# Kernel optimization log

Hardware: AMD Instinct MI355X
Metric: run time of the kernel (lower is better)

Reference implementation:

```python
import jax, jax.numpy as jnp
import numpy as np

B, S, D = 2, 2048, 2048
H, KV, HD = 16, 4, 128          # n_heads, n_kv_heads, head_dim = d_model // n_heads
R = H // KV                      # n_rep (GQA group size)
THETA = 500000.0


def _rotate_half(x):
    x1, x2 = jnp.split(x, 2, axis=-1)
    return jnp.concatenate([-x2, x1], axis=-1)


def _rope_cos_sin(position_ids):
    # inv_freq over even dims, outer with positions, duplicated (LLaMA-style)
    inv_freq = 1.0 / (THETA ** (jnp.arange(0, HD, 2, dtype=jnp.float32) / HD))
    freqs = position_ids.astype(jnp.float32)[..., None] * inv_freq  # (B, S, HD/2)
    emb = jnp.concatenate([freqs, freqs], axis=-1)                  # (B, S, HD)
    return jnp.cos(emb)[:, None], jnp.sin(emb)[:, None]             # (B, 1, S, HD)


def setup_inputs() -> dict:
    key = jax.random.key(0)
    ks = jax.random.split(key, 5)
    x = jax.random.normal(ks[0], (B, S, D), dtype=jnp.float32)
    wq = jax.random.normal(ks[1], (D, H * HD), dtype=jnp.float32) * (D ** -0.5)
    wk = jax.random.normal(ks[2], (D, KV * HD), dtype=jnp.float32) * (D ** -0.5)
    wv = jax.random.normal(ks[3], (D, KV * HD), dtype=jnp.float32) * (D ** -0.5)
    wo = jax.random.normal(ks[4], (H * HD, D), dtype=jnp.float32) * (D ** -0.5)
    causal = jnp.tril(jnp.ones((S, S), dtype=bool))
    attn_mask = jnp.where(causal, 0.0, -1e9).astype(jnp.float32)[None, None]  # (1,1,S,S)
    position_ids = jnp.tile(jnp.arange(S, dtype=jnp.int32)[None, :], (B, 1))
    return {"x": x, "wq": wq, "wk": wk, "wv": wv, "wo": wo,
            "attn_mask": attn_mask, "position_ids": position_ids}


def reference(x, wq, wk, wv, wo, attn_mask, position_ids):
    b, s, _ = x.shape
    # projections (bias-free Linear) + head split, (B, heads, S, HD)
    q = (x @ wq).reshape(b, s, H, HD).transpose(0, 2, 1, 3)
    k = (x @ wk).reshape(b, s, KV, HD).transpose(0, 2, 1, 3)
    v = (x @ wv).reshape(b, s, KV, HD).transpose(0, 2, 1, 3)
    cos, sin = _rope_cos_sin(position_ids)
    q = q * cos + _rotate_half(q) * sin
    k = k * cos + _rotate_half(k) * sin
    # GQA: group q heads (B, KV, R, S, HD); equivalent to repeat_interleave on K/V
    qg = q.reshape(b, KV, R, s, HD)
    scores = jnp.einsum('bgrsd,bgtd->bgrst', qg.astype(jnp.float32),
                        k.astype(jnp.float32)) / np.float32(np.sqrt(HD))
    scores = scores + attn_mask[:, :, None]          # (1,1,1,S,S) broadcast
    p = jax.nn.softmax(scores, axis=-1).astype(x.dtype)
    out = jnp.einsum('bgrst,bgtd->bgrsd', p, v)      # (B, KV, R, S, HD)
    out = out.reshape(b, H, s, HD).transpose(0, 2, 1, 3).reshape(b, s, H * HD)
    return out @ wo
```

## Files before the change

kernel.cpp:

```cpp
#include <hip/hip_runtime.h>
#include <hip/hip_bf16.h>
#include <math.h>

#define Bsz 2
#define Sq  2048
#define Dm  2048
#define Hn  16
#define KVn 4
#define HDn 128

typedef __attribute__((ext_vector_type(8))) short bf16x8;
typedef __attribute__((ext_vector_type(4))) float f32x4;

__device__ __forceinline__ short f2b(float f) {
    __hip_bfloat16 h = __float2bfloat16(f);
    return *reinterpret_cast<short*>(&h);
}
__device__ __forceinline__ float b2f(short s) {
    __hip_bfloat16 h = *reinterpret_cast<__hip_bfloat16*>(&s);
    return __bfloat162float(h);
}

#define NB_F2B 8192
#define NB_WC  10240
__global__ __launch_bounds__(256) void prep_kernel(
    const float* __restrict__ X, short* __restrict__ Y,
    const float* __restrict__ wq, const float* __restrict__ wk,
    const float* __restrict__ wv, const float* __restrict__ wo,
    short* __restrict__ wqkvT, short* __restrict__ woT)
{
    __shared__ float t[32][33];
    const int bid = blockIdx.x;
    const int tid = threadIdx.x;

    if (bid < NB_F2B) {
        const int i = bid * 256 + tid;
        float4 v = ((const float4*)X)[i];
        short4 o;
        o.x = f2b(v.x); o.y = f2b(v.y); o.z = f2b(v.z); o.w = f2b(v.w);
        ((short4*)Y)[i] = o;
        return;
    }

    const int wb = bid - NB_F2B;
    const int n0 = (wb % 160) * 32;
    const int k0 = (wb / 160) * 32;
    const int tx = tid & 31, ty = tid >> 5;

    const float* W; int Nsec, nloc; short* dst;
    if (n0 < 2048)      { W = wq; Nsec = 2048; nloc = n0;        dst = wqkvT + (size_t)n0 * Dm; }
    else if (n0 < 2560) { W = wk; Nsec = 512;  nloc = n0 - 2048; dst = wqkvT + (size_t)n0 * Dm; }
    else if (n0 < 3072) { W = wv; Nsec = 512;  nloc = n0 - 2560; dst = wqkvT + (size_t)n0 * Dm; }
    else                { W = wo; Nsec = 2048; nloc = n0 - 3072; dst = woT + (size_t)(n0 - 3072) * Dm; }

#pragma unroll
    for (int r = 0; r < 4; ++r) {
        const int row = ty + 8 * r;
        t[row][tx] = W[(size_t)(k0 + row) * Nsec + nloc + tx];
    }
    __syncthreads();
#pragma unroll
    for (int r = 0; r < 4; ++r) {
        const int row = ty + 8 * r;
        dst[(size_t)row * Dm + k0 + tx] = f2b(t[tx][row]);
    }
}

template <typename OT>
__global__ __launch_bounds__(256) void gemm_bt_kernel(
    const short* __restrict__ A, const short* __restrict__ Bt,
    OT* __restrict__ C, int M, int N, int K)
{
    __shared__ __align__(16) short As[128 * 64];
    __shared__ __align__(16) short Bs[128 * 64];

    const int tid  = threadIdx.x;
    const int w    = tid >> 6;
    const int lane = tid & 63;
    const int m16  = lane & 15;
    const int g4   = lane >> 4;
    const int wm   = w >> 1, wn = w & 1;

    const int nwg = gridDim.x * gridDim.y;
    const int lin = blockIdx.y * gridDim.x + blockIdx.x;
    const int qq  = nwg >> 3;
    const int sw  = (lin & 7) * qq + (lin >> 3);
    const int bx  = sw % gridDim.x;
    const int by  = sw / gridDim.x;

    const int row0 = by * 128;
    const int col0 = bx * 128;

    const short* Ab = A  + (size_t)row0 * K;
    const short* Bb = Bt + (size_t)col0 * K;

    const int trow = tid >> 3;
    const int soct = (tid & 7) ^ (trow & 7);

    f32x4 acc[4][4];
#pragma unroll
    for (int i = 0; i < 4; ++i)
#pragma unroll
        for (int j = 0; j < 4; ++j) acc[i][j] = (f32x4){0.f, 0.f, 0.f, 0.f};

    for (int k0 = 0; k0 < K; k0 += 64) {
#pragma unroll
        for (int r = 0; r < 4; ++r) {
            const short* gp = Ab + (size_t)(r * 32 + trow) * K + k0 + soct * 8;
            short* lp = &As[(size_t)(r * 256 + w * 64) * 8];
            __builtin_amdgcn_global_load_lds(
                (const __attribute__((address_space(1))) void*)gp,
                (__attribute__((address_space(3))) void*)lp, 16, 0, 0);
        }
#pragma unroll
        for (int r = 0; r < 4; ++r) {
            const short* gp = Bb + (size_t)(r * 32 + trow) * K + k0 + soct * 8;
            short* lp = &Bs[(size_t)(r * 256 + w * 64) * 8];
            __builtin_amdgcn_global_load_lds(
                (const __attribute__((address_space(1))) void*)gp,
                (__attribute__((address_space(3))) void*)lp, 16, 0, 0);
        }
        __syncthreads();

#pragma unroll
        for (int kc = 0; kc < 2; ++kc) {
            bf16x8 a[4], b[4];
            const int swz = (kc * 4 + g4) ^ (m16 & 7);
#pragma unroll
            for (int s = 0; s < 4; ++s) {
                const int rowA = wm * 64 + s * 16 + m16;
                a[s] = *(const bf16x8*)&As[rowA * 64 + swz * 8];
                const int rowB = wn * 64 + s * 16 + m16;
                b[s] = *(const bf16x8*)&Bs[rowB * 64 + swz * 8];
            }
#pragma unroll
            for (int i = 0; i < 4; ++i)
#pragma unroll
                for (int j = 0; j < 4; ++j)
                    acc[i][j] = __builtin_amdgcn_mfma_f32_16x16x32_bf16(
                        a[i], b[j], acc[i][j], 0, 0, 0);
        }
        __syncthreads();
    }

#pragma unroll
    for (int i = 0; i < 4; ++i) {
        const int mbase = row0 + wm * 64 + i * 16 + g4 * 4;
#pragma unroll
        for (int j = 0; j < 4; ++j) {
            const int n = col0 + wn * 64 + j * 16 + m16;
#pragma unroll
            for (int r = 0; r < 4; ++r) {
                if constexpr (sizeof(OT) == 2)
                    C[(size_t)(mbase + r) * N + n] = f2b(acc[i][j][r]);
                else
                    C[(size_t)(mbase + r) * N + n] = acc[i][j][r];
            }
        }
    }
}

#define NB_ROPE 1024
#define NB_VC   2048
__global__ __launch_bounds__(256) void rv_kernel(
    const short* __restrict__ C3b, short* __restrict__ Qb, short* __restrict__ Kb,
    short* __restrict__ Vt, const int* __restrict__ pos_ids, float qscale)
{
    __shared__ short tv[32][34];
    const int bid = blockIdx.x;
    const int tid = threadIdx.x;

    if (bid < NB_ROPE) {
        const int idx = bid * 256 + tid;
        const int i = idx & 63;
        int rest = idx >> 6;
        const int s = rest % Sq;
        const int b = rest / Sq;

        const int pos = pos_ids[b * Sq + s];
        const float e   = -(float)(2 * i) * (1.0f / (float)HDn);
        const float inv = exp2f(e * 18.931568569324174f);
        const float f   = (float)pos * inv;
        float sn, c;
        sincosf(f, &sn, &c);

        const short* src = C3b + ((size_t)(b * Sq + s)) * 3072;

#pragma unroll
        for (int h = 0; h < Hn; ++h) {
            const float x1 = b2f(src[h * HDn + i]);
            const float x2 = b2f(src[h * HDn + i + 64]);
            const size_t dst = (((size_t)b * Hn + h) * Sq + s) * HDn;
            Qb[dst + i]      = f2b((x1 * c - x2 * sn) * qscale);
            Qb[dst + i + 64] = f2b((x2 * c + x1 * sn) * qscale);
        }
#pragma unroll
        for (int h = 0; h < KVn; ++h) {
            const float x1 = b2f(src[2048 + h * HDn + i]);
            const float x2 = b2f(src[2048 + h * HDn + i + 64]);
            const size_t dst = (((size_t)b * KVn + h) * Sq + s) * HDn;
            Kb[dst + i]      = f2b(x1 * c - x2 * sn);
            Kb[dst + i + 64] = f2b(x2 * c + x1 * sn);
        }
        return;
    }

    const int lin = bid - NB_ROPE;
    const int bxv = lin & 63;
    const int rest = lin >> 6;
    const int byv = rest & 3;
    const int bk  = rest >> 2;
    const int b  = bk >> 2, kv = bk & 3;
    const int s0 = bxv * 32;
    const int d0 = byv * 32;
    const int tx = tid & 31, ty = tid >> 5;

#pragma unroll
    for (int r = 0; r < 4; ++r) {
        const int row = ty + 8 * r;
        tv[row][tx] = C3b[((size_t)(b * Sq + s0 + row)) * 3072 + 2560 + kv * HDn + d0 + tx];
    }
    __syncthreads();
#pragma unroll
    for (int r = 0; r < 4; ++r) {
        const int row = ty + 8 * r;
        Vt[((size_t)bk * HDn + d0 + row) * Sq + s0 + tx] = tv[tx][row];
    }
}

__global__ __launch_bounds__(256, 2) void fattn_kernel(
    const short* __restrict__ Qb, const short* __restrict__ Kb,
    const short* __restrict__ Vtb, short* __restrict__ AOb)
{
    __shared__ __align__(16) short Ks[2][64 * 128];
    __shared__ __align__(16) short Vs[2][128 * 64];

    const int tid  = threadIdx.x;
    const int w    = tid >> 6;
    const int lane = tid & 63;
    const int m16  = lane & 15;
    const int g4   = lane >> 4;

    const int i    = blockIdx.x;
    const int half = i >> 8;
    const int k4   = i & 15;
    const int p    = half ? k4 : 15 - k4;
    const int h    = (i >> 4) & 15;
    const int b    = i >> 8;
    const int kv   = h >> 2;

    const int htA = 31 - p, htB = p;
    const int nch = htA + 1;
    const int qA  = htA * 64 + w * 16;
    const int qB  = htB * 64 + w * 16;

    bf16x8 qfA[4], qfB[4];
    {
        const short* qpA = Qb + (((size_t)b * Hn + h) * Sq + qA + m16) * HDn + g4 * 8;
        const short* qpB = Qb + (((size_t)b * Hn + h) * Sq + qB + m16) * HDn + g4 * 8;
#pragma unroll
        for (int c = 0; c < 4; ++c) {
            qfA[c] = *(const bf16x8*)(qpA + c * 32);
            qfB[c] = *(const bf16x8*)(qpB + c * 32);
        }
    }

    const short* kbase = Kb  + ((size_t)b * KVn + kv) * Sq * HDn;
    const short* vbase = Vtb + ((size_t)b * KVn + kv) * (size_t)HDn * Sq;

    const short* gpK[4];
    const short* gpV[4];
#pragma unroll
    for (int r = 0; r < 4; ++r) {
        const int ci = r * 256 + tid;
        const int R  = ci >> 4, o = ci & 15;
        const int hf = (R >> 5) & 1, Rl = R & 31;
        const int phys = hf * 32 + ((Rl >> 2) & 3) * 8 + ((Rl >> 4) & 1) * 4 + (Rl & 3);
        gpK[r] = kbase + (size_t)phys * HDn + (o ^ (R & 7)) * 8;
        const int d = ci >> 3, ov = ci & 7;
        gpV[r] = vbase + (size_t)d * Sq + (ov ^ (d & 7)) * 8;
    }

    auto stage = [&](int ktE, int buf) {
#pragma unroll
        for (int r = 0; r < 4; ++r) {
            const short* gp = gpK[r] + (size_t)ktE * HDn;
            short* lp = &Ks[buf][(size_t)(r * 256 + w * 64) * 8];
            __builtin_amdgcn_global_load_lds(
                (const __attribute__((address_space(1))) void*)gp,
                (__attribute__((address_space(3))) void*)lp, 16, 0, 0);
        }
#pragma unroll
        for (int r = 0; r < 4; ++r) {
            const short* gp = gpV[r] + ktE;
            short* lp = &Vs[buf][(size_t)(r * 256 + w * 64) * 8];
            __builtin_amdgcn_global_load_lds(
                (const __attribute__((address_space(1))) void*)gp,
                (__attribute__((address_space(3))) void*)lp, 16, 0, 0);
        }
    };

    f32x4 OtA[8], OtB[8];
#pragma unroll
    for (int t = 0; t < 8; ++t) {
        OtA[t] = (f32x4){0.f, 0.f, 0.f, 0.f};
        OtB[t] = (f32x4){0.f, 0.f, 0.f, 0.f};
    }
    float mA = -1e30f, lA = 0.f, mB = -1e30f, lB = 0.f;

    stage(0, 0);
    int gpar = 0;

    for (int ch = 0; ch <= p; ++ch) {
        const int cur = gpar & 1; gpar ^= 1;
        const int kt  = ch << 6;

        __syncthreads();
        stage((ch + 1) << 6, cur ^ 1);

        const bool dgB = (ch == p);
        const short* KsC = Ks[cur];
        const short* VsC = Vs[cur];

        f32x4 sc0[4], sc1[4];
        __builtin_amdgcn_s_setprio(1);
#pragma unroll
        for (int f = 0; f < 4; ++f) {
            f32x4 a0 = (f32x4){0.f, 0.f, 0.f, 0.f};
            f32x4 a1 = (f32x4){0.f, 0.f, 0.f, 0.f};
            const int krow = f * 16 + m16;
#pragma unroll
            for (int c = 0; c < 4; ++c) {
                bf16x8 kf = *(const bf16x8*)&KsC[krow * 128 + (((c * 4 + g4) ^ (m16 & 7)) * 8)];
                a0 = __builtin_amdgcn_mfma_f32_16x16x32_bf16(kf, qfA[c], a0, 0, 0, 0);
                a1 = __builtin_amdgcn_mfma_f32_16x16x32_bf16(kf, qfB[c], a1, 0, 0, 0);
            }
            sc0[f] = a0; sc1[f] = a1;
        }
        __builtin_amdgcn_s_setprio(0);

        if (dgB) {
            const int qg = qB + m16;
#pragma unroll
            for (int f = 0; f < 4; ++f)
#pragma unroll
                for (int ii = 0; ii < 4; ++ii) {
                    const int kg = kt + (f >> 1) * 32 + g4 * 8 + (f & 1) * 4 + ii;
                    if (kg > qg) sc1[f][ii] = -1e30f;
                }
        }

        bf16x8 pf0[2], pf1[2];
        {
            float mx = sc0[0][0];
#pragma unroll
            for (int f = 0; f < 4; ++f)
#pragma unroll
                for (int ii = 0; ii < 4; ++ii) mx = fmaxf(mx, sc0[f][ii]);
            mx = fmaxf(mx, __shfl_xor(mx, 16));
            mx = fmaxf(mx, __shfl_xor(mx, 32));
            if (!__all(mx <= mA + 8.0f)) {
                const float nm = fmaxf(mA, mx);
                const float alpha = exp2f(mA - nm);
                mA = nm; lA *= alpha;
#pragma unroll
                for (int t = 0; t < 8; ++t)
#pragma unroll
                    for (int ii = 0; ii < 4; ++ii) OtA[t][ii] *= alpha;
            }
            float ps = 0.f;
#pragma unroll
            for (int f = 0; f < 4; ++f)
#pragma unroll
                for (int ii = 0; ii < 4; ++ii) {
                    sc0[f][ii] = exp2f(sc0[f][ii] - mA);
                    ps += sc0[f][ii];
                }
            ps += __shfl_xor(ps, 16);
            ps += __shfl_xor(ps, 32);
            lA += ps;
#pragma unroll
            for (int hf = 0; hf < 2; ++hf) {
                bf16x8 pk;
#pragma unroll
                for (int j8 = 0; j8 < 8; ++j8)
                    pk[j8] = f2b(j8 < 4 ? sc0[hf * 2][j8] : sc0[hf * 2 + 1][j8 - 4]);
                pf0[hf] = pk;
            }
        }
        {
            float mx = sc1[0][0];
#pragma unroll
            for (int f = 0; f < 4; ++f)
#pragma unroll
                for (int ii = 0; ii < 4; ++ii) mx = fmaxf(mx, sc1[f][ii]);
            mx = fmaxf(mx, __shfl_xor(mx, 16));
            mx = fmaxf(mx, __shfl_xor(mx, 32));
            if (!__all(mx <= mB + 8.0f)) {
                const float nm = fmaxf(mB, mx);
                const float alpha = exp2f(mB - nm);
                mB = nm; lB *= alpha;
#pragma unroll
                for (int t = 0; t < 8; ++t)
#pragma unroll
                    for (int ii = 0; ii < 4; ++ii) OtB[t][ii] *= alpha;
            }
            float ps = 0.f;
#pragma unroll
            for (int f = 0; f < 4; ++f)
#pragma unroll
                for (int ii = 0; ii < 4; ++ii) {
                    sc1[f][ii] = exp2f(sc1[f][ii] - mB);
                    ps += sc1[f][ii];
                }
            ps += __shfl_xor(ps, 16);
            ps += __shfl_xor(ps, 32);
            lB += ps;
#pragma unroll
            for (int hf = 0; hf < 2; ++hf) {
                bf16x8 pk;
#pragma unroll
                for (int j8 = 0; j8 < 8; ++j8)
                    pk[j8] = f2b(j8 < 4 ? sc1[hf * 2][j8] : sc1[hf * 2 + 1][j8 - 4]);
                pf1[hf] = pk;
            }
        }

        __builtin_amdgcn_s_setprio(1);
#pragma unroll
        for (int t = 0; t < 8; ++t) {
            const int d = t * 16 + m16;
            bf16x8 vfa = *(const bf16x8*)&VsC[d * 64 + ((g4 ^ (d & 7)) * 8)];
            bf16x8 vfb = *(const bf16x8*)&VsC[d * 64 + (((4 + g4) ^ (d & 7)) * 8)];
            OtA[t] = __builtin_amdgcn_mfma_f32_16x16x32_bf16(vfa, pf0[0], OtA[t], 0, 0, 0);
            OtA[t] = __builtin_amdgcn_mfma_f32_16x16x32_bf16(vfb, pf0[1], OtA[t], 0, 0, 0);
            OtB[t] = __builtin_amdgcn_mfma_f32_16x16x32_bf16(vfa, pf1[0], OtB[t], 0, 0, 0);
            OtB[t] = __builtin_amdgcn_mfma_f32_16x16x32_bf16(vfb, pf1[1], OtB[t], 0, 0, 0);
        }
        __builtin_amdgcn_s_setprio(0);
    }

    {
        const float inv = 1.0f / lB;
        short* op = AOb + ((size_t)(b * Sq + qB + m16)) * (Hn * HDn) + h * HDn + g4 * 4;
#pragma unroll
        for (int t = 0; t < 8; ++t) {
            short4 o;
            o.x = f2b(OtB[t][0] * inv);
            o.y = f2b(OtB[t][1] * inv);
            o.z = f2b(OtB[t][2] * inv);
            o.w = f2b(OtB[t][3] * inv);
            *(short4*)(op + t * 16) = o;
        }
    }

    for (int ch = p + 1; ch < nch; ++ch) {
        const int cur = gpar & 1; gpar ^= 1;
        const int kt  = ch << 6;

        __syncthreads();
        if (ch + 1 < nch) stage((ch + 1) << 6, cur ^ 1);

        const bool dgA = (ch == nch - 1);
        const short* KsC = Ks[cur];
        const short* VsC = Vs[cur];

        f32x4 sc[4];
        __builtin_amdgcn_s_setprio(1);
#pragma unroll
        for (int f = 0; f < 4; ++f) {
            f32x4 a = (f32x4){0.f, 0.f, 0.f, 0.f};
            const int krow = f * 16 + m16;
#pragma unroll
            for (int c = 0; c < 4; ++c) {
                bf16x8 kf = *(const bf16x8*)&KsC[krow * 128 + (((c * 4 + g4) ^ (m16 & 7)) * 8)];
                a = __builtin_amdgcn_mfma_f32_16x16x32_bf16(kf, qfA[c], a, 0, 0, 0);
            }
            sc[f] = a;
        }
        __builtin_amdgcn_s_setprio(0);

        if (dgA) {
            const int qg = qA + m16;
#pragma unroll
            for (int f = 0; f < 4; ++f)
#pragma unroll
                for (int ii = 0; ii < 4; ++ii) {
                    const int kg = kt + (f >> 1) * 32 + g4 * 8 + (f & 1) * 4 + ii;
                    if (kg > qg) sc[f][ii] = -1e30f;
                }
        }

        float mx = sc[0][0];
#pragma unroll
        for (int f = 0; f < 4; ++f)
#pragma unroll
            for (int ii = 0; ii < 4; ++ii) mx = fmaxf(mx, sc[f][ii]);
        mx = fmaxf(mx, __shfl_xor(mx, 16));
        mx = fmaxf(mx, __shfl_xor(mx, 32));
        if (!__all(mx <= mA + 8.0f)) {
            const float nm = fmaxf(mA, mx);
            const float alpha = exp2f(mA - nm);
            mA = nm; lA *= alpha;
#pragma unroll
            for (int t = 0; t < 8; ++t)
#pragma unroll
                for (int ii = 0; ii < 4; ++ii) OtA[t][ii] *= alpha;
        }
        float ps = 0.f;
#pragma unroll
        for (int f = 0; f < 4; ++f)
#pragma unroll
            for (int ii = 0; ii < 4; ++ii) {
                sc[f][ii] = exp2f(sc[f][ii] - mA);
                ps += sc[f][ii];
            }
        ps += __shfl_xor(ps, 16);
        ps += __shfl_xor(ps, 32);
        lA += ps;

        bf16x8 pf[2];
#pragma unroll
        for (int hf = 0; hf < 2; ++hf) {
            bf16x8 pk;
#pragma unroll
            for (int j8 = 0; j8 < 8; ++j8)
                pk[j8] = f2b(j8 < 4 ? sc[hf * 2][j8] : sc[hf * 2 + 1][j8 - 4]);
            pf[hf] = pk;
        }

        __builtin_amdgcn_s_setprio(1);
#pragma unroll
        for (int t = 0; t < 8; ++t) {
            const int d = t * 16 + m16;
            bf16x8 vfa = *(const bf16x8*)&VsC[d * 64 + ((g4 ^ (d & 7)) * 8)];
            bf16x8 vfb = *(const bf16x8*)&VsC[d * 64 + (((4 + g4) ^ (d & 7)) * 8)];
            OtA[t] = __builtin_amdgcn_mfma_f32_16x16x32_bf16(vfa, pf[0], OtA[t], 0, 0, 0);
            OtA[t] = __builtin_amdgcn_mfma_f32_16x16x32_bf16(vfb, pf[1], OtA[t], 0, 0, 0);
        }
        __builtin_amdgcn_s_setprio(0);
    }

    {
        const float inv = 1.0f / lA;
        short* op = AOb + ((size_t)(b * Sq + qA + m16)) * (Hn * HDn) + h * HDn + g4 * 4;
#pragma unroll
        for (int t = 0; t < 8; ++t) {
            short4 o;
            o.x = f2b(OtA[t][0] * inv);
            o.y = f2b(OtA[t][1] * inv);
            o.z = f2b(OtA[t][2] * inv);
            o.w = f2b(OtA[t][3] * inv);
            *(short4*)(op + t * 16) = o;
        }
    }
}

extern "C" void kernel_launch(void* const* d_in, const int* in_sizes, int n_in,
                              void* d_out, int out_size, void* d_ws, size_t ws_size,
                              hipStream_t stream)
{
    const float* x   = (const float*)d_in[0];
    const float* wq  = (const float*)d_in[1];
    const float* wk  = (const float*)d_in[2];
    const float* wv  = (const float*)d_in[3];
    const float* wo  = (const float*)d_in[4];
    const int* pos   = (const int*)d_in[6];
    float* out = (float*)d_out;

    const int M = Bsz * Sq;
    const size_t nX  = (size_t)M * Dm;

    short* xb    = (short*)d_ws;
    short* wqkvT = xb + nX;
    short* woT   = wqkvT + (size_t)3072 * Dm;
    short* C3b   = woT + (size_t)Dm * Dm;
    short* Qb    = C3b + (size_t)M * 3072;
    short* Kb    = Qb + nX;
    short* Vtb   = Kb + (size_t)Bsz * KVn * Sq * HDn;
    short* AOb   = Vtb + (size_t)Bsz * KVn * Sq * HDn;

    prep_kernel<<<NB_F2B + NB_WC, 256, 0, stream>>>(
        x, xb, wq, wk, wv, wo, wqkvT, woT);

    gemm_bt_kernel<short><<<dim3(3072 / 128, M / 128), 256, 0, stream>>>(
        xb, wqkvT, C3b, M, 3072, Dm);

    {
        const float qscale = 0.08838834764831845f * 1.4426950408889634f;
        rv_kernel<<<NB_ROPE + NB_VC, 256, 0, stream>>>(
            C3b, Qb, Kb, Vtb, pos, qscale);
    }

    fattn_kernel<<<Bsz * Hn * 16, 256, 0, stream>>>(Qb, Kb, Vtb, AOb);

    gemm_bt_kernel<float><<<dim3(Dm / 128, M / 128), 256, 0, stream>>>(
        AOb, woT, out, M, Dm, Dm);
}
```

Baseline: 317.3 us.

## Fuse RoPE into QKV GEMM epilogue and use packed bf16 conversion

The QKV GEMM epilogue now applies RoPE and the Q scale directly. It writes Q and K in head-major layout and writes only V to a narrow buffer, removing the separate rope pass over the full 3072-wide intermediate. The B-fragment column mapping is permuted so each wave holds both rotate-half partners. Cos/sin tables are precomputed in the prep kernel. The attention kernel switches probability packing to v_cvt_pk_bf16_f32, and the epilogue stores stay scattered 2-byte writes.

```diff
diff --git a/kernel.cpp b/kernel.cpp
--- a/kernel.cpp
+++ b/kernel.cpp
@@ -11,6 +11,7 @@
 
 typedef __attribute__((ext_vector_type(8))) short bf16x8;
 typedef __attribute__((ext_vector_type(4))) float f32x4;
+typedef __attribute__((ext_vector_type(4))) unsigned int u32x4;
 
 __device__ __forceinline__ short f2b(float f) {
     __hip_bfloat16 h = __float2bfloat16(f);
@@ -20,14 +21,21 @@
     __hip_bfloat16 h = *reinterpret_cast<__hip_bfloat16*>(&s);
     return __bfloat162float(h);
 }
+__device__ __forceinline__ unsigned pk2(float lo, float hh) {
+    unsigned r;
+    asm("v_cvt_pk_bf16_f32 %0, %1, %2" : "=v"(r) : "v"(lo), "v"(hh));
+    return r;
+}
 
 #define NB_F2B 8192
 #define NB_WC  10240
+#define NB_TCS 1024
 __global__ __launch_bounds__(256) void prep_kernel(
     const float* __restrict__ X, short* __restrict__ Y,
     const float* __restrict__ wq, const float* __restrict__ wk,
     const float* __restrict__ wv, const float* __restrict__ wo,
-    short* __restrict__ wqkvT, short* __restrict__ woT)
+    short* __restrict__ wqkvT, short* __restrict__ woT,
+    const int* __restrict__ pos_ids, float* __restrict__ tcs)
 {
     __shared__ float t[32][33];
     const int bid = blockIdx.x;
@@ -41,6 +49,19 @@
         ((short4*)Y)[i] = o;
         return;
     }
+    if (bid >= NB_F2B + NB_WC) {
+        const int idx = (bid - NB_F2B - NB_WC) * 256 + tid;
+        const int d = idx >> 12, gr = idx & 4095;
+        const int pos = pos_ids[gr];
+        const float e   = -(float)(2 * d) * (1.0f / (float)HDn);
+        const float inv = exp2f(e * 18.931568569324174f);
+        const float f   = (float)pos * inv;
+        float sn, c;
+        sincosf(f, &sn, &c);
+        float2 cs; cs.x = c; cs.y = sn;
+        ((float2*)tcs)[idx] = cs;
+        return;
+    }
 
     const int wb = bid - NB_F2B;
     const int n0 = (wb % 160) * 32;
@@ -66,14 +87,15 @@
     }
 }
 
-template <typename OT>
-__global__ __launch_bounds__(256) void gemm_bt_kernel(
+__global__ __launch_bounds__(256) void gemm_qkv_kernel(
     const short* __restrict__ A, const short* __restrict__ Bt,
-    OT* __restrict__ C, int M, int N, int K)
+    short* __restrict__ Qb, short* __restrict__ Kbp, short* __restrict__ C3v,
+    const float* __restrict__ tcs, float qscale)
 {
     __shared__ __align__(16) short As[128 * 64];
     __shared__ __align__(16) short Bs[128 * 64];
 
+    const int K = Dm, Mg = Bsz * Sq;
     const int tid  = threadIdx.x;
     const int w    = tid >> 6;
     const int lane = tid & 63;
@@ -130,7 +152,7 @@
             for (int s = 0; s < 4; ++s) {
                 const int rowA = wm * 64 + s * 16 + m16;
                 a[s] = *(const bf16x8*)&As[rowA * 64 + swz * 8];
-                const int rowB = wn * 64 + s * 16 + m16;
+                const int rowB = (s & 1) * 64 + wn * 32 + (s >> 1) * 16 + m16;
                 b[s] = *(const bf16x8*)&Bs[rowB * 64 + swz * 8];
             }
 #pragma unroll
@@ -143,88 +165,161 @@
         __syncthreads();
     }
 
+    const int dloc = wn * 32 + m16;
+    if (bx < 20) {
+        const bool isQ = bx < 16;
+        const int hh = isQ ? bx : bx - 16;
+        const int NH = isQ ? Hn : KVn;
+        short* Yb = isQ ? Qb : Kbp;
+        const float scale = isQ ? qscale : 1.0f;
+#pragma unroll
+        for (int i = 0; i < 4; ++i) {
+            const int gr0 = row0 + wm * 64 + i * 16 + g4 * 4;
+            const int bb = gr0 >> 11, ss = gr0 & 2047;
+            short* op = Yb + (((size_t)bb * NH + hh) * Sq + ss) * HDn;
+#pragma unroll
+            for (int jp = 0; jp < 2; ++jp) {
+                const int d = dloc + jp * 16;
+                const float4 t0 = *(const float4*)&tcs[((size_t)d * 4096 + gr0) * 2];
+                const float4 t1 = *(const float4*)&tcs[((size_t)d * 4096 + gr0 + 2) * 2];
+                const float cc0 = t0.x, sn0 = t0.y, cc1 = t0.z, sn1 = t0.w;
+                const float cc2 = t1.x, sn2 = t1.y, cc3 = t1.z, sn3 = t1.w;
+#pragma unroll
+                for (int r = 0; r < 4; ++r) {
+                    const float cc = (r == 0) ? cc0 : (r == 1) ? cc1 : (r == 2) ? cc2 : cc3;
+                    const float sn = (r == 0) ? sn0 : (r == 1) ? sn1 : (r == 2) ? sn2 : sn3;
+                    const float x1 = acc[i][2 * jp][r];
+                    const float x2 = acc[i][2 * jp + 1][r];
+                    op[(size_t)r * HDn + d]      = f2b((x1 * cc - x2 * sn) * scale);
+                    op[(size_t)r * HDn + d + 64] = f2b((x2 * cc + x1 * sn) * scale);
+                }
+            }
+        }
+    } else {
+        const int kvh = bx - 20;
+#pragma unroll
+        for (int i = 0; i < 4; ++i) {
+            const int gr0 = row0 + wm * 64 + i * 16 + g4 * 4;
+#pragma unroll
+            for (int j = 0; j < 4; ++j) {
+                const int col = (j & 1) * 64 + wn * 32 + (j >> 1) * 16 + m16;
+#pragma unroll
+                for (int r = 0; r < 4; ++r)
+                    C3v[(size_t)(gr0 + r) * 512 + kvh * 128 + col] = f2b(acc[i][j][r]);
+            }
+        }
+    }
+}
+
+__global__ __launch_bounds__(256) void gemm_o_kernel(
+    const short* __restrict__ A, const short* __restrict__ Bt,
+    float* __restrict__ C, int M, int N, int K)
+{
+    __shared__ __align__(16) short As[128 * 64];
+    __shared__ __align__(16) short Bs[128 * 64];
+
+    const int tid  = threadIdx.x;
+    const int w    = tid >> 6;
+    const int lane = tid & 63;
+    const int m16  = lane & 15;
+    const int g4   = lane >> 4;
+    const int wm   = w >> 1, wn = w & 1;
+
+    const int nwg = gridDim.x * gridDim.y;
+    const int lin = blockIdx.y * gridDim.x + blockIdx.x;
+    const int qq  = nwg >> 3;
+    const int sw  = (lin & 7) * qq + (lin >> 3);
+    const int bx  = sw % gridDim.x;
+    const int by  = sw / gridDim.x;
+
+    const int row0 = by * 128;
+    const int col0 = bx * 128;
+
+    const short* Ab = A  + (size_t)row0 * K;
+    const short* Bb = Bt + (size_t)col0 * K;
+
+    const int trow = tid >> 3;
+    const int soct = (tid & 7) ^ (trow & 7);
+
+    f32x4 acc[4][4];
+#pragma unroll
+    for (int i = 0; i < 4; ++i)
+#pragma unroll
+        for (int j = 0; j < 4; ++j) acc[i][j] = (f32x4){0.f, 0.f, 0.f, 0.f};
+
+    for (int k0 = 0; k0 < K; k0 += 64) {
+#pragma unroll
+        for (int r = 0; r < 4; ++r) {
+            const short* gp = Ab + (size_t)(r * 32 + trow) * K + k0 + soct * 8;
+            short* lp = &As[(size_t)(r * 256 + w * 64) * 8];
+            __builtin_amdgcn_global_load_lds(
+                (const __attribute__((address_space(1))) void*)gp,
+                (__attribute__((address_space(3))) void*)lp, 16, 0, 0);
+        }
+#pragma unroll
+        for (int r = 0; r < 4; ++r) {
+            const short* gp = Bb + (size_t)(r * 32 + trow) * K + k0 + soct * 8;
+            short* lp = &Bs[(size_t)(r * 256 + w * 64) * 8];
+            __builtin_amdgcn_global_load_lds(
+                (const __attribute__((address_space(1))) void*)gp,
+                (__attribute__((address_space(3))) void*)lp, 16, 0, 0);
+        }
+        __syncthreads();
+
+#pragma unroll
+        for (int kc = 0; kc < 2; ++kc) {
+            bf16x8 a[4], b[4];
+            const int swz = (kc * 4 + g4) ^ (m16 & 7);
+#pragma unroll
+            for (int s = 0; s < 4; ++s) {
+                const int rowA = wm * 64 + s * 16 + m16;
+                a[s] = *(const bf16x8*)&As[rowA * 64 + swz * 8];
+                const int rowB = (s & 1) * 64 + wn * 32 + (s >> 1) * 16 + m16;
+                b[s] = *(const bf16x8*)&Bs[rowB * 64 + swz * 8];
+            }
+#pragma unroll
+            for (int i = 0; i < 4; ++i)
+#pragma unroll
+                for (int j = 0; j < 4; ++j)
+                    acc[i][j] = __builtin_amdgcn_mfma_f32_16x16x32_bf16(
+                        a[i], b[j], acc[i][j], 0, 0, 0);
+        }
+        __syncthreads();
+    }
+
 #pragma unroll
     for (int i = 0; i < 4; ++i) {
         const int mbase = row0 + wm * 64 + i * 16 + g4 * 4;
 #pragma unroll
         for (int j = 0; j < 4; ++j) {
-            const int n = col0 + wn * 64 + j * 16 + m16;
-#pragma unroll
-            for (int r = 0; r < 4; ++r) {
-                if constexpr (sizeof(OT) == 2)
-                    C[(size_t)(mbase + r) * N + n] = f2b(acc[i][j][r]);
-                else
-                    C[(size_t)(mbase + r) * N + n] = acc[i][j][r];
-            }
-        }
-    }
-}
-
-#define NB_ROPE 1024
-#define NB_VC   2048
-__global__ __launch_bounds__(256) void rv_kernel(
-    const short* __restrict__ C3b, short* __restrict__ Qb, short* __restrict__ Kb,
-    short* __restrict__ Vt, const int* __restrict__ pos_ids, float qscale)
+            const int n = col0 + (j & 1) * 64 + wn * 32 + (j >> 1) * 16 + m16;
+#pragma unroll
+            for (int r = 0; r < 4; ++r)
+                C[(size_t)(mbase + r) * N + n] = acc[i][j][r];
+        }
+    }
+}
+
+__global__ __launch_bounds__(256) void vconv_kernel(
+    const short* __restrict__ C3v, short* __restrict__ Vt)
 {
-    __shared__ short tv[32][34];
-    const int bid = blockIdx.x;
-    const int tid = threadIdx.x;
-
-    if (bid < NB_ROPE) {
-        const int idx = bid * 256 + tid;
-        const int i = idx & 63;
-        int rest = idx >> 6;
-        const int s = rest % Sq;
-        const int b = rest / Sq;
-
-        const int pos = pos_ids[b * Sq + s];
-        const float e   = -(float)(2 * i) * (1.0f / (float)HDn);
-        const float inv = exp2f(e * 18.931568569324174f);
-        const float f   = (float)pos * inv;
-        float sn, c;
-        sincosf(f, &sn, &c);
-
-        const short* src = C3b + ((size_t)(b * Sq + s)) * 3072;
-
-#pragma unroll
-        for (int h = 0; h < Hn; ++h) {
-            const float x1 = b2f(src[h * HDn + i]);
-            const float x2 = b2f(src[h * HDn + i + 64]);
-            const size_t dst = (((size_t)b * Hn + h) * Sq + s) * HDn;
-            Qb[dst + i]      = f2b((x1 * c - x2 * sn) * qscale);
-            Qb[dst + i + 64] = f2b((x2 * c + x1 * sn) * qscale);
-        }
-#pragma unroll
-        for (int h = 0; h < KVn; ++h) {
-            const float x1 = b2f(src[2048 + h * HDn + i]);
-            const float x2 = b2f(src[2048 + h * HDn + i + 64]);
-            const size_t dst = (((size_t)b * KVn + h) * Sq + s) * HDn;
-            Kb[dst + i]      = f2b(x1 * c - x2 * sn);
-            Kb[dst + i + 64] = f2b(x2 * c + x1 * sn);
-        }
-        return;
-    }
-
-    const int lin = bid - NB_ROPE;
-    const int bxv = lin & 63;
-    const int rest = lin >> 6;
-    const int byv = rest & 3;
-    const int bk  = rest >> 2;
+    __shared__ short t[32][34];
+    const int bk = blockIdx.z;
     const int b  = bk >> 2, kv = bk & 3;
-    const int s0 = bxv * 32;
-    const int d0 = byv * 32;
-    const int tx = tid & 31, ty = tid >> 5;
+    const int s0 = blockIdx.x * 32;
+    const int d0 = blockIdx.y * 32;
+    const int tx = threadIdx.x, ty = threadIdx.y;
 
 #pragma unroll
     for (int r = 0; r < 4; ++r) {
         const int row = ty + 8 * r;
-        tv[row][tx] = C3b[((size_t)(b * Sq + s0 + row)) * 3072 + 2560 + kv * HDn + d0 + tx];
+        t[row][tx] = C3v[((size_t)(b * Sq + s0 + row)) * 512 + kv * 128 + d0 + tx];
     }
     __syncthreads();
 #pragma unroll
     for (int r = 0; r < 4; ++r) {
         const int row = ty + 8 * r;
-        Vt[((size_t)bk * HDn + d0 + row) * Sq + s0 + tx] = tv[tx][row];
+        Vt[((size_t)bk * HDn + d0 + row) * Sq + s0 + tx] = t[tx][row];
     }
 }
 
@@ -249,10 +344,10 @@
     const int b    = i >> 8;
     const int kv   = h >> 2;
 
-    const int htA = 31 - p, htB = p;
+    const int htA = 31 - p;
     const int nch = htA + 1;
     const int qA  = htA * 64 + w * 16;
-    const int qB  = htB * 64 + w * 16;
+    const int qB  = p * 64 + w * 16;
 
     bf16x8 qfA[4], qfB[4];
     {
@@ -379,14 +474,13 @@
             ps += __shfl_xor(ps, 16);
             ps += __shfl_xor(ps, 32);
             lA += ps;
-#pragma unroll
-            for (int hf = 0; hf < 2; ++hf) {
-                bf16x8 pk;
-#pragma unroll
-                for (int j8 = 0; j8 < 8; ++j8)
-                    pk[j8] = f2b(j8 < 4 ? sc0[hf * 2][j8] : sc0[hf * 2 + 1][j8 - 4]);
-                pf0[hf] = pk;
-            }
+            u32x4 u;
+            u[0] = pk2(sc0[0][0], sc0[0][1]); u[1] = pk2(sc0[0][2], sc0[0][3]);
+            u[2] = pk2(sc0[1][0], sc0[1][1]); u[3] = pk2(sc0[1][2], sc0[1][3]);
+            pf0[0] = *(bf16x8*)&u;
+            u[0] = pk2(sc0[2][0], sc0[2][1]); u[1] = pk2(sc0[2][2], sc0[2][3]);
+            u[2] = pk2(sc0[3][0], sc0[3][1]); u[3] = pk2(sc0[3][2], sc0[3][3]);
+            pf0[1] = *(bf16x8*)&u;
         }
         {
             float mx = sc1[0][0];
@@ -416,14 +510,13 @@
             ps += __shfl_xor(ps, 16);
             ps += __shfl_xor(ps, 32);
             lB += ps;
-#pragma unroll
-            for (int hf = 0; hf < 2; ++hf) {
-                bf16x8 pk;
-#pragma unroll
-                for (int j8 = 0; j8 < 8; ++j8)
-                    pk[j8] = f2b(j8 < 4 ? sc1[hf * 2][j8] : sc1[hf * 2 + 1][j8 - 4]);
-                pf1[hf] = pk;
-            }
+            u32x4 u;
+            u[0] = pk2(sc1[0][0], sc1[0][1]); u[1] = pk2(sc1[0][2], sc1[0][3]);
+            u[2] = pk2(sc1[1][0], sc1[1][1]); u[3] = pk2(sc1[1][2], sc1[1][3]);
+            pf1[0] = *(bf16x8*)&u;
+            u[0] = pk2(sc1[2][0], sc1[2][1]); u[1] = pk2(sc1[2][2], sc1[2][3]);
+            u[2] = pk2(sc1[3][0], sc1[3][1]); u[3] = pk2(sc1[3][2], sc1[3][3]);
+            pf1[1] = *(bf16x8*)&u;
         }
 
         __builtin_amdgcn_s_setprio(1);
@@ -520,13 +613,14 @@
         lA += ps;
 
         bf16x8 pf[2];
-#pragma unroll
-        for (int hf = 0; hf < 2; ++hf) {
-            bf16x8 pk;
-#pragma unroll
-            for (int j8 = 0; j8 < 8; ++j8)
-                pk[j8] = f2b(j8 < 4 ? sc[hf * 2][j8] : sc[hf * 2 + 1][j8 - 4]);
-            pf[hf] = pk;
+        {
+            u32x4 u;
+            u[0] = pk2(sc[0][0], sc[0][1]); u[1] = pk2(sc[0][2], sc[0][3]);
+            u[2] = pk2(sc[1][0], sc[1][1]); u[3] = pk2(sc[1][2], sc[1][3]);
+            pf[0] = *(bf16x8*)&u;
+            u[0] = pk2(sc[2][0], sc[2][1]); u[1] = pk2(sc[2][2], sc[2][3]);
+            u[2] = pk2(sc[3][0], sc[3][1]); u[3] = pk2(sc[3][2], sc[3][3]);
+            pf[1] = *(bf16x8*)&u;
         }
 
         __builtin_amdgcn_s_setprio(1);
@@ -574,26 +668,26 @@
     short* xb    = (short*)d_ws;
     short* wqkvT = xb + nX;
     short* woT   = wqkvT + (size_t)3072 * Dm;
-    short* C3b   = woT + (size_t)Dm * Dm;
-    short* Qb    = C3b + (size_t)M * 3072;
+    short* C3v   = woT + (size_t)Dm * Dm;
+    short* Qb    = C3v + (size_t)M * 512;
     short* Kb    = Qb + nX;
     short* Vtb   = Kb + (size_t)Bsz * KVn * Sq * HDn;
     short* AOb   = Vtb + (size_t)Bsz * KVn * Sq * HDn;
-
-    prep_kernel<<<NB_F2B + NB_WC, 256, 0, stream>>>(
-        x, xb, wq, wk, wv, wo, wqkvT, woT);
-
-    gemm_bt_kernel<short><<<dim3(3072 / 128, M / 128), 256, 0, stream>>>(
-        xb, wqkvT, C3b, M, 3072, Dm);
-
-    {
-        const float qscale = 0.08838834764831845f * 1.4426950408889634f;
-        rv_kernel<<<NB_ROPE + NB_VC, 256, 0, stream>>>(
-            C3b, Qb, Kb, Vtb, pos, qscale);
-    }
+    float* tcs   = (float*)(AOb + nX);
+
+    const float qscale = 0.08838834764831845f * 1.4426950408889634f;
+
+    prep_kernel<<<NB_F2B + NB_WC + NB_TCS, 256, 0, stream>>>(
+        x, xb, wq, wk, wv, wo, wqkvT, woT, pos, tcs);
+
+    gemm_qkv_kernel<<<dim3(3072 / 128, M / 128), 256, 0, stream>>>(
+        xb, wqkvT, Qb, Kb, C3v, tcs, qscale);
+
+    vconv_kernel<<<dim3(Sq / 32, HDn / 32, Bsz * KVn), dim3(32, 8), 0, stream>>>(
+        C3v, Vtb);
 
     fattn_kernel<<<Bsz * Hn * 16, 256, 0, stream>>>(Qb, Kb, Vtb, AOb);
 
-    gemm_bt_kernel<float><<<dim3(Dm / 128, M / 128), 256, 0, stream>>>(
+    gemm_o_kernel<<<dim3(Dm / 128, M / 128), 256, 0, stream>>>(
         AOb, woT, out, M, Dm, Dm);
 }
```

Result: no change. 320.4 us (+1.0%).
